# Kernel optimization log

Measured on AMD Instinct MI355X. Metric: run time of the kernel, lower is better.

Reference implementation:

```python
import jax, jax.numpy as jnp
import numpy as np

P = 1.0  # Yager t-norm exponent (tnorm_p)


def _patches(x, k):
    # x: [B, C, H, W] -> [B, C*k*k, Ho, Wo], feature ordering (c, kh, kw) like torch unfold
    B, C, H, W = x.shape
    Ho, Wo = H - k + 1, W - k + 1
    cols = [x[:, :, i:i + Ho, j:j + Wo] for i in range(k) for j in range(k)]
    p = jnp.stack(cols, axis=2)  # [B, C, k*k, Ho, Wo]
    return p.reshape(B, C * k * k, Ho, Wo)


def _max_yager2d(x, w, p):
    # Fuzzy conv: Yager t-norm T(a,b)=max(0, 1-((1-a)^p+(1-b)^p)^(1/p)) between each
    # patch element and kernel weight, aggregated with max over the receptive field.
    O, C, k, _ = w.shape
    pat = _patches(x, k)                       # [B, L, Ho, Wo], L = C*k*k
    wf = w.reshape(O, -1)                      # [O, L]
    a = 1.0 - pat[:, None]                     # [B, 1, L, Ho, Wo]
    b = 1.0 - wf[None, :, :, None, None]       # [1, O, L, 1, 1]
    t = jnp.maximum(0.0, 1.0 - (a ** p + b ** p) ** (1.0 / p))
    return jnp.max(t, axis=2)                  # [B, O, Ho, Wo]


def _maxpool2(x):
    return jax.lax.reduce_window(x, -jnp.inf, jax.lax.max,
                                 (1, 1, 2, 2), (1, 1, 2, 2), 'VALID')


def setup_inputs() -> dict:
    key = jax.random.key(0)
    k1, k2, k3, k4, k5, k6, k7 = jax.random.split(key, 7)
    B = 128
    inputs = jax.random.uniform(k1, (B, 3, 32, 32), dtype=jnp.float32)
    # fuzzy kernels are membership values in [0,1]
    w1 = jax.random.uniform(k2, (6, 3, 5, 5), dtype=jnp.float32)
    w2 = jax.random.uniform(k3, (16, 6, 5, 5), dtype=jnp.float32)
    w3 = jax.random.uniform(k4, (120, 16, 5, 5), dtype=jnp.float32)
    wd = jax.random.normal(k5, (120, 84), dtype=jnp.float32) * 0.1  # DenseDefuzzy weights
    wf = jax.random.normal(k6, (84, 10), dtype=jnp.float32) * 0.1   # fc5 weight
    bf = jax.random.normal(k7, (10,), dtype=jnp.float32) * 0.01     # fc5 bias
    return {"inputs": inputs, "w1": w1, "w2": w2, "w3": w3,
            "wd": wd, "wf": wf, "bf": bf}


def reference(inputs, w1, w2, w3, wd, wf, bf):
    x = _maxpool2(_max_yager2d(inputs, w1, P))   # [B,6,14,14]
    x = _maxpool2(_max_yager2d(x, w2, P))        # [B,16,5,5]
    x = _max_yager2d(x, w3, P)                   # [B,120,1,1]
    x = x.reshape(x.shape[0], -1)                # [B,120]
    x = jnp.tanh(x @ wd)                         # DenseDefuzzy (unnormalized) + tanh
    return jax.nn.log_softmax(x @ wf + bf, axis=-1)
```

## Files before the change

kernel.cpp:

```cpp
#include <hip/hip_runtime.h>
#include <math.h>


#define NT 1024
#define ROWS 34
#define PLANE (32 * ROWS)

__device__ __forceinline__ void dilate_row(const float* __restrict__ raw,
                                           int r, float* __restrict__ dst) {
    const int rA = (r > 0) ? r - 1 : 0;
    const int rB = (r < 5) ? r : 4;
    float t0 = fmaxf(raw[rA * 5 + 0], raw[rB * 5 + 0]);
    float t1 = fmaxf(raw[rA * 5 + 1], raw[rB * 5 + 1]);
    float t2 = fmaxf(raw[rA * 5 + 2], raw[rB * 5 + 2]);
    float t3 = fmaxf(raw[rA * 5 + 3], raw[rB * 5 + 3]);
    float t4 = fmaxf(raw[rA * 5 + 4], raw[rB * 5 + 4]);
    float2* d = (float2*)dst;
    d[0] = make_float2(t0, fmaxf(t0, t1));
    d[1] = make_float2(fmaxf(t1, t2), fmaxf(t2, t3));
    d[2] = make_float2(fmaxf(t3, t4), t4);
}

__global__ __launch_bounds__(NT) void fused_lenet(
    const float* __restrict__ x,
    const float* __restrict__ w1,
    const float* __restrict__ w2,
    const float* __restrict__ w3,
    const float* __restrict__ wd,
    const float* __restrict__ wf,
    const float* __restrict__ bfv,
    float* __restrict__ out)
{
    const int img = blockIdx.x;
    const int tid = threadIdx.x;

    __shared__ float s_in[3 * PLANE];
    __shared__ float s_w1d[648];
    __shared__ float s_w2d[3456];
    __shared__ float s_wf[850];
    __shared__ unsigned s_a1u[1176];
    __shared__ unsigned s_a2u[400];
    __shared__ float s_a3[120];
    __shared__ float s_a4[84];

    float4 w3p[13];

    {
        const float2* src = (const float2*)(x + img * 3072);
        for (int i = tid; i < 1536; i += NT) {
            const int c = i >> 9, rem = i & 511, r = rem >> 4, col2 = rem & 15;
            ((float2*)s_in)[c * (PLANE / 2) + r * (ROWS / 2) + col2] = src[i];
        }
        if (tid < 420) ((float2*)s_wf)[tid] = ((const float2*)wf)[tid];
        if (tid >= 428 && tid < 438) s_wf[840 + tid - 428] = bfv[tid - 428];
        for (int i = tid; i < 1176; i += NT) s_a1u[i] = 0u;
        if (tid < 400) s_a2u[tid] = 0u;
        if (tid >= 320 && tid < 428) {
            const int e = tid - 320;
            const int occ = e / 6, r = e - occ * 6;
            dilate_row(w1 + occ * 25, r, s_w1d + occ * 36 + r * 6);
        }
        if (tid >= 448) {
            const int e = tid - 448;
            const int occ = e / 6, r = e - occ * 6;
            dilate_row(w2 + occ * 25, r, s_w2d + occ * 36 + r * 6);
        }
    }
    __syncthreads();

    if (tid < 336) {
        const int c = tid / 112;
        const int r = tid - c * 112;
        const int ocg = r / 56;
        const int r2 = r - ocg * 56;
        const int py = r2 >> 2;
        const int s = (r2 >> 1) & 1;
        const int h = r2 & 1;
        float acc[3][7];
        #pragma unroll
        for (int o = 0; o < 3; ++o)
            #pragma unroll
            for (int j = 0; j < 7; ++j) acc[o][j] = -1e30f;
        const float* xbase = s_in + c * PLANE + (2 * py + 3 * h) * ROWS + 14 * s;
        #pragma unroll
        for (int u = 0; u < 3; ++u) {
            float xv[18];
            #pragma unroll
            for (int i2 = 0; i2 < 9; ++i2)
                ((float2*)xv)[i2] = ((const float2*)(xbase + u * ROWS))[i2];
            #pragma unroll
            for (int o = 0; o < 3; ++o) {
                const float* wbase =
                    s_w1d + ((ocg * 3 + o) * 3 + c) * 36 + h * 18 + u * 6;
                float wv[6];
                #pragma unroll
                for (int i2 = 0; i2 < 3; ++i2)
                    ((float2*)wv)[i2] = ((const float2*)wbase)[i2];
                #pragma unroll
                for (int j = 0; j < 7; ++j) {
                    #pragma unroll
                    for (int ux = 0; ux < 6; ++ux)
                        acc[o][j] = fmaxf(acc[o][j], xv[2 * j + ux] + wv[ux]);
                }
            }
        }
        #pragma unroll
        for (int o = 0; o < 3; ++o) {
            const int obase = (ocg * 3 + o) * 196 + py * 14 + 7 * s;
            #pragma unroll
            for (int j = 0; j < 7; ++j) {
                const float rl = fmaxf(acc[o][j] - 1.0f, 0.0f);
                atomicMax(&s_a1u[obase + j], __float_as_uint(rl));
            }
        }
    }
    if (tid < 960) {
        const int o = tid >> 3, q = tid & 7;
        const float4* wv = (const float4*)(w3 + o * 400);
        #pragma unroll
        for (int i = 0; i < 13; ++i) {
            int l = q + 8 * i; if (l > 99) l = 99;
            w3p[i] = wv[l];
        }
    }
    __syncthreads();

    if (tid < 240) {
        const int ocq = tid / 60;
        const int r = tid - ocq * 60;
        const int py = r / 12;
        const int r2 = r - py * 12;
        const int c = r2 >> 1;
        const int h = r2 & 1;
        float acc[4][5];
        #pragma unroll
        for (int o = 0; o < 4; ++o)
            #pragma unroll
            for (int j = 0; j < 5; ++j) acc[o][j] = -1e30f;
        const float* a1f = (const float*)s_a1u;
        const float* xbase = a1f + c * 196 + (2 * py + 3 * h) * 14;
        #pragma unroll
        for (int u = 0; u < 3; ++u) {
            float xv[14];
            #pragma unroll
            for (int i2 = 0; i2 < 7; ++i2)
                ((float2*)xv)[i2] = ((const float2*)(xbase + u * 14))[i2];
            #pragma unroll
            for (int o = 0; o < 4; ++o) {
                const float* wbase =
                    s_w2d + ((ocq * 4 + o) * 6 + c) * 36 + h * 18 + u * 6;
                float wv[6];
                #pragma unroll
                for (int i2 = 0; i2 < 3; ++i2)
                    ((float2*)wv)[i2] = ((const float2*)wbase)[i2];
                #pragma unroll
                for (int j = 0; j < 5; ++j) {
                    #pragma unroll
                    for (int ux = 0; ux < 6; ++ux)
                        acc[o][j] = fmaxf(acc[o][j], xv[2 * j + ux] + wv[ux]);
                }
            }
        }
        #pragma unroll
        for (int o = 0; o < 4; ++o) {
            const int obase = (ocq * 4 + o) * 25 + py * 5;
            #pragma unroll
            for (int j = 0; j < 5; ++j) {
                const float rl = fmaxf(acc[o][j] - 1.0f, 0.0f);
                atomicMax(&s_a2u[obase + j], __float_as_uint(rl));
            }
        }
    }
    float wdp[15];
    if (tid < 672) {
        const int o = tid >> 3, q = tid & 7;
        #pragma unroll
        for (int i = 0; i < 15; ++i)
            wdp[i] = wd[(q * 15 + i) * 84 + o];
    }
    __syncthreads();

    if (tid < 960) {
        const int o = tid >> 3, q = tid & 7;
        const float4* av = (const float4*)(const float*)s_a2u;
        float m = -1e30f;
        #pragma unroll
        for (int i = 0; i < 13; ++i) {
            int l = q + 8 * i; if (l > 99) l = 99;
            const float4 a = av[l];
            const float4 w = w3p[i];
            m = fmaxf(m, fmaxf(fmaxf(a.x + w.x, a.y + w.y),
                               fmaxf(a.z + w.z, a.w + w.w)));
        }
        m = fmaxf(m, __shfl_xor(m, 1));
        m = fmaxf(m, __shfl_xor(m, 2));
        m = fmaxf(m, __shfl_xor(m, 4));
        if (q == 0) s_a3[o] = fmaxf(m - 1.0f, 0.0f);
    }
    __syncthreads();

    if (tid < 672) {
        const int o = tid >> 3, q = tid & 7;
        float acc = 0.0f;
        #pragma unroll
        for (int i = 0; i < 15; ++i)
            acc = fmaf(s_a3[q * 15 + i], wdp[i], acc);
        acc += __shfl_xor(acc, 1);
        acc += __shfl_xor(acc, 2);
        acc += __shfl_xor(acc, 4);
        if (q == 0)
            s_a4[o] = 1.0f - 2.0f / (__expf(2.0f * acc) + 1.0f);
    }
    __syncthreads();

    if (tid < 64) {
        float acc = 0.0f;
        if (tid < 40) {
            const int o = tid >> 2, q = tid & 3;
            #pragma unroll 7
            for (int i = 0; i < 21; ++i) {
                const int k = q * 21 + i;
                acc = fmaf(s_a4[k], s_wf[k * 10 + o], acc);
            }
            acc += __shfl_xor(acc, 1);
            acc += __shfl_xor(acc, 2);
            acc += s_wf[840 + o];
        }
        const float lg = __shfl(acc, (tid < 10) ? tid * 4 : 0);
        if (tid < 16) {
            float v = (tid < 10) ? lg : -1e30f;
            #pragma unroll
            for (int d = 1; d < 16; d <<= 1)
                v = fmaxf(v, __shfl_xor(v, d));
            float e = (tid < 10) ? __expf(lg - v) : 0.0f;
            float ssum = e;
            #pragma unroll
            for (int d = 1; d < 16; d <<= 1)
                ssum += __shfl_xor(ssum, d);
            if (tid < 10)
                out[img * 10 + tid] = lg - v - __logf(ssum);
        }
    }
}

extern "C" void kernel_launch(void* const* d_in, const int* in_sizes, int n_in,
                              void* d_out, int out_size, void* d_ws, size_t ws_size,
                              hipStream_t stream) {
    const float* x   = (const float*)d_in[0];
    const float* w1  = (const float*)d_in[1];
    const float* w2  = (const float*)d_in[2];
    const float* w3  = (const float*)d_in[3];
    const float* wd  = (const float*)d_in[4];
    const float* wf  = (const float*)d_in[5];
    const float* bfv = (const float*)d_in[6];
    float* out = (float*)d_out;

    const int B = in_sizes[0] / (3 * 32 * 32);
    fused_lenet<<<dim3(B), dim3(NT), 0, stream>>>(
        x, w1, w2, w3, wd, wf, bfv, out);
}
```

Before: 73.59 us.

## Spread conv1 over more threads and merge half-window partials with DPP

Conv1 is re-partitioned from 336 threads to 1008 threads by also splitting the three kernel rows (u) across threads, with the two row-halves (h) placed on adjacent lanes. Those lane pairs are combined with a DPP quad-permute max, so only one lane issues the shared-memory atomicMax, which halves the atomics from the pair. Conv2 gets the same DPP pair combine, and both stages reorder the max into a tree to shorten dependency chains. The extra threads each redo the x loads, and the per-u split still needs atomics to merge the partial results across rows.

```diff
diff --git a/kernel.cpp b/kernel.cpp
--- a/kernel.cpp
+++ b/kernel.cpp
@@ -5,6 +5,12 @@
 #define NT 1024
 #define ROWS 34
 #define PLANE (32 * ROWS)
+
+__device__ __forceinline__ float dpp_pairmax(float v) {
+    int p = __builtin_amdgcn_update_dpp(0, __float_as_int(v),
+                                        0xB1, 0xF, 0xF, true);
+    return fmaxf(v, __int_as_float(p));
+}
 
 __device__ __forceinline__ void dilate_row(const float* __restrict__ raw,
                                            int r, float* __restrict__ dst) {
@@ -68,49 +74,51 @@
     }
     __syncthreads();
 
-    if (tid < 336) {
-        const int c = tid / 112;
-        const int r = tid - c * 112;
-        const int ocg = r / 56;
-        const int r2 = r - ocg * 56;
-        const int py = r2 >> 2;
-        const int s = (r2 >> 1) & 1;
-        const int h = r2 & 1;
-        float acc[3][7];
-        #pragma unroll
-        for (int o = 0; o < 3; ++o)
-            #pragma unroll
-            for (int j = 0; j < 7; ++j) acc[o][j] = -1e30f;
-        const float* xbase = s_in + c * PLANE + (2 * py + 3 * h) * ROWS + 14 * s;
-        #pragma unroll
-        for (int u = 0; u < 3; ++u) {
-            float xv[18];
-            #pragma unroll
-            for (int i2 = 0; i2 < 9; ++i2)
-                ((float2*)xv)[i2] = ((const float2*)(xbase + u * ROWS))[i2];
-            #pragma unroll
-            for (int o = 0; o < 3; ++o) {
-                const float* wbase =
-                    s_w1d + ((ocg * 3 + o) * 3 + c) * 36 + h * 18 + u * 6;
-                float wv[6];
-                #pragma unroll
-                for (int i2 = 0; i2 < 3; ++i2)
-                    ((float2*)wv)[i2] = ((const float2*)wbase)[i2];
+    if (tid < 1008) {
+        const int h = tid & 1;
+        const int q = tid >> 1;
+        const int g = q / 56;
+        const int inner = q - g * 56;
+        const int c = g / 3;
+        const int u = g - c * 3;
+        const int ocg = inner / 28;
+        const int it = inner - ocg * 28;
+        const int py = it >> 1;
+        const int s = it & 1;
+        const float* xbase =
+            s_in + c * PLANE + (2 * py + 3 * h + u) * ROWS + 14 * s;
+        float xv[18];
+        #pragma unroll
+        for (int iv = 0; iv < 9; ++iv)
+            ((float2*)xv)[iv] = ((const float2*)xbase)[iv];
+        #pragma unroll
+        for (int o = 0; o < 3; ++o) {
+            const float* wbase =
+                s_w1d + ((ocg * 3 + o) * 3 + c) * 36 + (3 * h + u) * 6;
+            float wv[6];
+            #pragma unroll
+            for (int iv = 0; iv < 3; ++iv)
+                ((float2*)wv)[iv] = ((const float2*)wbase)[iv];
+            float mrow[7];
+            #pragma unroll
+            for (int j = 0; j < 7; ++j) {
+                const float t0 = xv[2 * j + 0] + wv[0];
+                const float t1 = xv[2 * j + 1] + wv[1];
+                const float t2 = xv[2 * j + 2] + wv[2];
+                const float t3 = xv[2 * j + 3] + wv[3];
+                const float t4 = xv[2 * j + 4] + wv[4];
+                const float t5 = xv[2 * j + 5] + wv[5];
+                const float m1 = fmaxf(fmaxf(t0, t1), t2);
+                const float m2 = fmaxf(fmaxf(t3, t4), t5);
+                mrow[j] = dpp_pairmax(fmaxf(m1, m2));
+            }
+            if (h == 0) {
+                const int obase = (ocg * 3 + o) * 196 + py * 14 + 7 * s;
                 #pragma unroll
                 for (int j = 0; j < 7; ++j) {
-                    #pragma unroll
-                    for (int ux = 0; ux < 6; ++ux)
-                        acc[o][j] = fmaxf(acc[o][j], xv[2 * j + ux] + wv[ux]);
+                    const float rl = fmaxf(mrow[j] - 1.0f, 0.0f);
+                    atomicMax(&s_a1u[obase + j], __float_as_uint(rl));
                 }
-            }
-        }
-        #pragma unroll
-        for (int o = 0; o < 3; ++o) {
-            const int obase = (ocg * 3 + o) * 196 + py * 14 + 7 * s;
-            #pragma unroll
-            for (int j = 0; j < 7; ++j) {
-                const float rl = fmaxf(acc[o][j] - 1.0f, 0.0f);
-                atomicMax(&s_a1u[obase + j], __float_as_uint(rl));
             }
         }
     }
@@ -143,31 +151,42 @@
         for (int u = 0; u < 3; ++u) {
             float xv[14];
             #pragma unroll
-            for (int i2 = 0; i2 < 7; ++i2)
-                ((float2*)xv)[i2] = ((const float2*)(xbase + u * 14))[i2];
+            for (int iv = 0; iv < 7; ++iv)
+                ((float2*)xv)[iv] = ((const float2*)(xbase + u * 14))[iv];
             #pragma unroll
             for (int o = 0; o < 4; ++o) {
                 const float* wbase =
                     s_w2d + ((ocq * 4 + o) * 6 + c) * 36 + h * 18 + u * 6;
                 float wv[6];
                 #pragma unroll
-                for (int i2 = 0; i2 < 3; ++i2)
-                    ((float2*)wv)[i2] = ((const float2*)wbase)[i2];
+                for (int iv = 0; iv < 3; ++iv)
+                    ((float2*)wv)[iv] = ((const float2*)wbase)[iv];
                 #pragma unroll
                 for (int j = 0; j < 5; ++j) {
-                    #pragma unroll
-                    for (int ux = 0; ux < 6; ++ux)
-                        acc[o][j] = fmaxf(acc[o][j], xv[2 * j + ux] + wv[ux]);
+                    const float t0 = xv[2 * j + 0] + wv[0];
+                    const float t1 = xv[2 * j + 1] + wv[1];
+                    const float t2 = xv[2 * j + 2] + wv[2];
+                    const float t3 = xv[2 * j + 3] + wv[3];
+                    const float t4 = xv[2 * j + 4] + wv[4];
+                    const float t5 = xv[2 * j + 5] + wv[5];
+                    const float m1 = fmaxf(fmaxf(t0, t1), t2);
+                    const float m2 = fmaxf(fmaxf(t3, t4), t5);
+                    acc[o][j] = fmaxf(acc[o][j], fmaxf(m1, m2));
                 }
             }
         }
         #pragma unroll
         for (int o = 0; o < 4; ++o) {
-            const int obase = (ocq * 4 + o) * 25 + py * 5;
-            #pragma unroll
-            for (int j = 0; j < 5; ++j) {
-                const float rl = fmaxf(acc[o][j] - 1.0f, 0.0f);
-                atomicMax(&s_a2u[obase + j], __float_as_uint(rl));
+            float comb[5];
+            #pragma unroll
+            for (int j = 0; j < 5; ++j) comb[j] = dpp_pairmax(acc[o][j]);
+            if (h == 0) {
+                const int obase = (ocq * 4 + o) * 25 + py * 5;
+                #pragma unroll
+                for (int j = 0; j < 5; ++j) {
+                    const float rl = fmaxf(comb[j] - 1.0f, 0.0f);
+                    atomicMax(&s_a2u[obase + j], __float_as_uint(rl));
+                }
             }
         }
     }
```

Result: slower. 89.68 us (+21.9%).
